# Optimization experiments

Hardware: AMD Instinct MI355X
Metric: run time of the kernel (lower is better)

## Reference

```python
import jax, jax.numpy as jnp
import numpy as np

N_FFT = 512
HOP = 256
FS = 16000
D_INTER = 0.04
C_SOUND = 343.0
SOURCE_NUM = 2
EST_NUM = 4      # TF snapshots for the spatial covariance
T_START = 120    # starting frame of the snapshots
EPS = 1e-8
N_ANGLES = 361   # theta in [-90, 90] deg
T_SAMPLES = 3200000
N_MICS = 4


def _stft(xc):
    """xc: (C, T) real -> X: (C, F, n_frames) complex64.
    Matches torch.stft(center=True, pad_mode='reflect', onesided=True)
    with window = hann(N_FFT, periodic=True) ** 0.5.
    """
    n = jnp.arange(N_FFT, dtype=xc.dtype)
    win = jnp.sqrt(0.5 * (1.0 - jnp.cos(2.0 * jnp.pi * n / N_FFT)))  # hann^0.5
    pad = N_FFT // 2
    xp = jnp.pad(xc, ((0, 0), (pad, pad)), mode='reflect')
    n_frames = 1 + xc.shape[1] // HOP
    idx = jnp.arange(n_frames)[:, None] * HOP + jnp.arange(N_FFT)[None, :]
    frames = xp[:, idx] * win                     # (C, n_frames, N_FFT)
    X = jnp.fft.rfft(frames, axis=-1)             # (C, n_frames, F)
    return jnp.swapaxes(X, 1, 2)                  # (C, F, n_frames)


def setup_inputs() -> dict:
    key = jax.random.key(0)
    x = jax.random.normal(key, (T_SAMPLES, N_MICS), dtype=jnp.float32)
    return {"x": x}


def reference(x) -> jnp.ndarray:
    # ---- multi-channel STFT ----
    X = _stft(x.T)                                # (M, F, T_frames) complex64
    M = X.shape[0]

    # ---- spatial covariance from EST_NUM snapshots (vectorized over bins) ----
    Xs = X[:, :, T_START:T_START + EST_NUM]       # (M, F, EST_NUM)
    spt = jnp.einsum('mft,nft->fmn', Xs, jnp.conj(Xs)) / EST_NUM  # (F, M, M) Hermitian

    # ---- noise subspace via Hermitian eigendecomposition ----
    # eigh returns ascending eigenvalues; take the M-SOURCE_NUM smallest
    # (noise) eigenvectors, i.e. descending order then columns SOURCE_NUM:.
    _, V = jnp.linalg.eigh(spt)                   # (F, M, M)
    noise = V[:, :, ::-1][:, :, SOURCE_NUM:]      # (F, M, M-SOURCE_NUM)

    # ---- spatial spectrum, fully batched over all 361 angles ----
    f_analog = jnp.linspace(0.0, FS / 2, N_FFT // 2 + 1, dtype=jnp.float32)
    theta = jnp.deg2rad(jnp.linspace(-90.0, 90.0, N_ANGLES, dtype=jnp.float32))
    mics = jnp.arange(M, dtype=jnp.float32)
    # phase: (A, F, M)
    phase = (2.0 * jnp.pi * D_INTER / C_SOUND) * (
        jnp.sin(theta)[:, None, None] * f_analog[None, :, None] * mics[None, None, :]
    )
    steer = jnp.exp(-1j * phase).astype(jnp.complex64)            # (A, F, M)
    mid = jnp.einsum('afm,fmk->afk', steer, noise)                # (A, F, K)
    val = jnp.sum(mid.real ** 2 + mid.imag ** 2, axis=-1)         # (A, F)
    spt_spec = jnp.mean(1.0 / (val + EPS), axis=1)                # (A,)
    return spt_spec
```

## Files before the change

kernel.cpp:

```cpp
#include <hip/hip_runtime.h>
#include <math.h>

#define NFFT   512
#define HOP    256
#define NFREQ  257
#define NMIC   4
#define NEST   4
#define TSTART 120
#define NANG   361

static constexpr double PI_D = 3.14159265358979323846;
static constexpr float  PI_F = 3.14159265358979323846f;

__global__ __launch_bounds__(512)
void stft_kernel(const float* __restrict__ x,
                 float* __restrict__ part_re,
                 float* __restrict__ part_im) {
    int b = blockIdx.x;
    int chunk = b >> 4;
    int m = (b >> 2) & 3;
    int t = b & 3;
    int tid = threadIdx.x;

    __shared__ float ct[512];
    __shared__ float st[512];
    __shared__ float v[128];

    {
        float ang = (2.0f * PI_F / 512.0f) * (float)tid;
        float s, c;
        sincosf(ang, &s, &c);
        ct[tid] = c;
        st[tid] = s;
    }
    if (tid < 128) {
        int n = chunk * 128 + tid;
        long base = ((long)(TSTART + t - 1) * HOP) * NMIC + m;
        v[tid] = x[base + (long)n * NMIC] * sinf(PI_F * (float)n / 512.0f);
    }
    __syncthreads();

    int f = tid;
    if (f >= NFREQ) return;
    int n0 = chunk * 128;
    int k = (f * n0) & 511;
    float re = 0.0f, im = 0.0f;
#pragma unroll 4
    for (int j = 0; j < 128; ++j) {
        float vn = v[j];
        re += vn * ct[k];
        im -= vn * st[k];
        k = (k + f) & 511;
    }
    int id = f * 16 + m * 4 + t;
    part_re[chunk * 4112 + id] = re;
    part_im[chunk * 4112 + id] = im;
}

__global__ __launch_bounds__(64)
void eig_kernel(const float* __restrict__ part_re,
                const float* __restrict__ part_im,
                double* __restrict__ pre,
                double* __restrict__ pim) {
    int f = blockIdx.x * blockDim.x + threadIdx.x;
    if (f >= NFREQ) return;

    double Xr[4][4], Xi[4][4];
#pragma unroll
    for (int m = 0; m < 4; ++m)
#pragma unroll
        for (int t = 0; t < 4; ++t) {
            int id = f * 16 + m * 4 + t;
            Xr[m][t] = (double)part_re[id] + (double)part_re[4112 + id]
                     + (double)part_re[2 * 4112 + id] + (double)part_re[3 * 4112 + id];
            Xi[m][t] = (double)part_im[id] + (double)part_im[4112 + id]
                     + (double)part_im[2 * 4112 + id] + (double)part_im[3 * 4112 + id];
        }

    double Ar[4][4], Ai[4][4];
#pragma unroll
    for (int m = 0; m < 4; ++m)
#pragma unroll
        for (int n = 0; n < 4; ++n) {
            double rr = 0.0, ii = 0.0;
#pragma unroll
            for (int t = 0; t < 4; ++t) {
                rr += Xr[m][t] * Xr[n][t] + Xi[m][t] * Xi[n][t];
                ii += Xi[m][t] * Xr[n][t] - Xr[m][t] * Xi[n][t];
            }
            Ar[m][n] = rr;
            Ai[m][n] = ii;
        }

    double Vr[4][4] = {{1,0,0,0},{0,1,0,0},{0,0,1,0},{0,0,0,1}};
    double Vi[4][4] = {{0,0,0,0},{0,0,0,0},{0,0,0,0},{0,0,0,0}};

    for (int sweep = 0; sweep < 6; ++sweep) {
#pragma unroll
        for (int p = 0; p < 3; ++p)
#pragma unroll
            for (int q = p + 1; q < 4; ++q) {
                double ar = Ar[p][q], ai = Ai[p][q];
                double rmag = sqrt(ar * ar + ai * ai);
                if (rmag < 1e-280) continue;
                double inv = 1.0 / rmag;
                double er = ar * inv, ei = ai * inv;
                double tau = (Ar[q][q] - Ar[p][p]) * (0.5 * inv);
                double t_ = (tau >= 0.0 ? 1.0 : -1.0) /
                            (fabs(tau) + sqrt(1.0 + tau * tau));
                double c = 1.0 / sqrt(1.0 + t_ * t_);
                double s = t_ * c;
#pragma unroll
                for (int k = 0; k < 4; ++k) {
                    double apr = Ar[k][p], api = Ai[k][p];
                    double aqr = Ar[k][q], aqi = Ai[k][q];
                    double tr = er * aqr + ei * aqi;
                    double ti = er * aqi - ei * aqr;
                    Ar[k][p] = c * apr - s * tr;
                    Ai[k][p] = c * api - s * ti;
                    double ur = er * apr - ei * api;
                    double ui = er * api + ei * apr;
                    Ar[k][q] = s * ur + c * aqr;
                    Ai[k][q] = s * ui + c * aqi;
                }
#pragma unroll
                for (int k = 0; k < 4; ++k) {
                    double apr = Ar[p][k], api = Ai[p][k];
                    double aqr = Ar[q][k], aqi = Ai[q][k];
                    double tr = er * aqr - ei * aqi;
                    double ti = er * aqi + ei * aqr;
                    Ar[p][k] = c * apr - s * tr;
                    Ai[p][k] = c * api - s * ti;
                    double ur = er * apr + ei * api;
                    double ui = er * api - ei * apr;
                    Ar[q][k] = s * ur + c * aqr;
                    Ai[q][k] = s * ui + c * aqi;
                }
#pragma unroll
                for (int k = 0; k < 4; ++k) {
                    double apr = Vr[k][p], api = Vi[k][p];
                    double aqr = Vr[k][q], aqi = Vi[k][q];
                    double tr = er * aqr + ei * aqi;
                    double ti = er * aqi - ei * aqr;
                    Vr[k][p] = c * apr - s * tr;
                    Vi[k][p] = c * api - s * ti;
                    double ur = er * apr - ei * api;
                    double ui = er * api + ei * apr;
                    Vr[k][q] = s * ur + c * aqr;
                    Vi[k][q] = s * ui + c * aqi;
                }
            }
    }

    double dd[4] = {Ar[0][0], Ar[1][1], Ar[2][2], Ar[3][3]};
    double w[4];
#pragma unroll
    for (int j = 0; j < 4; ++j) {
        int rank = 0;
#pragma unroll
        for (int k = 0; k < 4; ++k) {
            if (k == j) continue;
            bool less = (dd[k] < dd[j]) || (dd[k] == dd[j] && k < j);
            rank += less ? 1 : 0;
        }
        w[j] = (rank < 2) ? 1.0 : 0.0;
    }

#pragma unroll
    for (int m = 0; m < 4; ++m)
#pragma unroll
        for (int n = 0; n < 4; ++n) {
            double rr = 0.0, ii = 0.0;
#pragma unroll
            for (int j = 0; j < 4; ++j) {
                rr += w[j] * (Vr[m][j] * Vr[n][j] + Vi[m][j] * Vi[n][j]);
                ii += w[j] * (Vi[m][j] * Vr[n][j] - Vr[m][j] * Vi[n][j]);
            }
            pre[f * 16 + m * 4 + n] = rr;
            pim[f * 16 + m * 4 + n] = ii;
        }
}

__global__ __launch_bounds__(512)
void music_kernel(const double* __restrict__ pre,
                  const double* __restrict__ pim,
                  float* __restrict__ out) {
    int a = blockIdx.x;
    int f = threadIdx.x;
    double r = 0.0;
    if (f < NFREQ) {
        double theta = (-90.0 + 0.5 * (double)a) * PI_D / 180.0;
        double freq = 31.25 * (double)f;
        double phi = 2.0 * PI_D * 0.04 / 343.0 * sin(theta) * freq;
        const double* Pr = pre + f * 16;
        const double* Pi = pim + f * 16;
        double s1, c1;
        sincos(phi, &s1, &c1);
        double c2 = c1 * c1 - s1 * s1;
        double s2 = 2.0 * s1 * c1;
        double c3 = c1 * c2 - s1 * s2;
        double s3 = s1 * c2 + c1 * s2;
        double val = Pr[0] + Pr[5] + Pr[10] + Pr[15]
            + 2.0 * ( c1 * (Pr[1] + Pr[6] + Pr[11]) - s1 * (Pi[1] + Pi[6] + Pi[11])
                    + c2 * (Pr[2] + Pr[7])          - s2 * (Pi[2] + Pi[7])
                    + c3 * Pr[3]                    - s3 * Pi[3] );
        r = 1.0 / (val + 1e-8);
    }
    __shared__ double sm[512];
    sm[threadIdx.x] = r;
    __syncthreads();
    for (int st = 256; st > 0; st >>= 1) {
        if (threadIdx.x < st) sm[threadIdx.x] += sm[threadIdx.x + st];
        __syncthreads();
    }
    if (threadIdx.x == 0) out[a] = (float)(sm[0] / (double)NFREQ);
}

extern "C" void kernel_launch(void* const* d_in, const int* in_sizes, int n_in,
                              void* d_out, int out_size, void* d_ws, size_t ws_size,
                              hipStream_t stream) {
    const float* x = (const float*)d_in[0];
    float* out = (float*)d_out;

    float*  part_re = (float*)d_ws;
    float*  part_im = part_re + 4 * 4112;
    double* pre     = (double*)((char*)d_ws + 2 * 4 * 4112 * sizeof(float));
    double* pim     = pre + 4112;

    stft_kernel<<<64, 512, 0, stream>>>(x, part_re, part_im);
    eig_kernel<<<(NFREQ + 63) / 64, 64, 0, stream>>>(part_re, part_im, pre, pim);
    music_kernel<<<NANG, 512, 0, stream>>>(pre, pim, out);
}
```

Baseline: 115.8 us.

## Switch eig and MUSIC to fp32, compact coefficients, use wave shuffle reductions

Converts the Jacobi eigensolver and the spatial spectrum kernel from double to single precision, replacing a branchy skip with select-based masking. The eig kernel now emits 7 diagonal-sum coefficients per bin instead of the full 4x4 projector, so the MUSIC kernel loads two float4s per bin. The MUSIC block shrinks to 320 threads and reduces with wave shuffles rather than a shared-memory tree, and STFT twiddles are packed into float2. The fp32 Jacobi with near-degenerate covariance (rank 4 from 4 snapshots) risks accuracy loss in the noise subspace.

```diff
diff --git a/kernel.cpp b/kernel.cpp
--- a/kernel.cpp
+++ b/kernel.cpp
@@ -5,7 +5,6 @@
 #define HOP    256
 #define NFREQ  257
 #define NMIC   4
-#define NEST   4
 #define TSTART 120
 #define NANG   361
 
@@ -22,16 +21,14 @@
     int t = b & 3;
     int tid = threadIdx.x;
 
-    __shared__ float ct[512];
-    __shared__ float st[512];
-    __shared__ float v[128];
+    __shared__ float2 tw[512];
+    __shared__ float  v[128];
 
     {
         float ang = (2.0f * PI_F / 512.0f) * (float)tid;
         float s, c;
         sincosf(ang, &s, &c);
-        ct[tid] = c;
-        st[tid] = s;
+        tw[tid] = make_float2(c, s);
     }
     if (tid < 128) {
         int n = chunk * 128 + tid;
@@ -42,14 +39,14 @@
 
     int f = tid;
     if (f >= NFREQ) return;
-    int n0 = chunk * 128;
-    int k = (f * n0) & 511;
+    int k = (f * (chunk * 128)) & 511;
     float re = 0.0f, im = 0.0f;
 #pragma unroll 4
     for (int j = 0; j < 128; ++j) {
         float vn = v[j];
-        re += vn * ct[k];
-        im -= vn * st[k];
+        float2 cs = tw[k];
+        re += vn * cs.x;
+        im -= vn * cs.y;
         k = (k + f) & 511;
     }
     int id = f * 16 + m * 4 + t;
@@ -60,29 +57,28 @@
 __global__ __launch_bounds__(64)
 void eig_kernel(const float* __restrict__ part_re,
                 const float* __restrict__ part_im,
-                double* __restrict__ pre,
-                double* __restrict__ pim) {
+                float* __restrict__ coef) {
     int f = blockIdx.x * blockDim.x + threadIdx.x;
     if (f >= NFREQ) return;
 
-    double Xr[4][4], Xi[4][4];
+    float Xr[4][4], Xi[4][4];
 #pragma unroll
     for (int m = 0; m < 4; ++m)
 #pragma unroll
         for (int t = 0; t < 4; ++t) {
             int id = f * 16 + m * 4 + t;
-            Xr[m][t] = (double)part_re[id] + (double)part_re[4112 + id]
-                     + (double)part_re[2 * 4112 + id] + (double)part_re[3 * 4112 + id];
-            Xi[m][t] = (double)part_im[id] + (double)part_im[4112 + id]
-                     + (double)part_im[2 * 4112 + id] + (double)part_im[3 * 4112 + id];
+            Xr[m][t] = part_re[id] + part_re[4112 + id]
+                     + part_re[2 * 4112 + id] + part_re[3 * 4112 + id];
+            Xi[m][t] = part_im[id] + part_im[4112 + id]
+                     + part_im[2 * 4112 + id] + part_im[3 * 4112 + id];
         }
 
-    double Ar[4][4], Ai[4][4];
+    float Ar[4][4], Ai[4][4];
 #pragma unroll
     for (int m = 0; m < 4; ++m)
 #pragma unroll
         for (int n = 0; n < 4; ++n) {
-            double rr = 0.0, ii = 0.0;
+            float rr = 0.0f, ii = 0.0f;
 #pragma unroll
             for (int t = 0; t < 4; ++t) {
                 rr += Xr[m][t] * Xr[n][t] + Xi[m][t] * Xi[n][t];
@@ -92,68 +88,69 @@
             Ai[m][n] = ii;
         }
 
-    double Vr[4][4] = {{1,0,0,0},{0,1,0,0},{0,0,1,0},{0,0,0,1}};
-    double Vi[4][4] = {{0,0,0,0},{0,0,0,0},{0,0,0,0},{0,0,0,0}};
+    float Vr[4][4] = {{1,0,0,0},{0,1,0,0},{0,0,1,0},{0,0,0,1}};
+    float Vi[4][4] = {{0,0,0,0},{0,0,0,0},{0,0,0,0},{0,0,0,0}};
 
     for (int sweep = 0; sweep < 6; ++sweep) {
 #pragma unroll
         for (int p = 0; p < 3; ++p)
 #pragma unroll
             for (int q = p + 1; q < 4; ++q) {
-                double ar = Ar[p][q], ai = Ai[p][q];
-                double rmag = sqrt(ar * ar + ai * ai);
-                if (rmag < 1e-280) continue;
-                double inv = 1.0 / rmag;
-                double er = ar * inv, ei = ai * inv;
-                double tau = (Ar[q][q] - Ar[p][p]) * (0.5 * inv);
-                double t_ = (tau >= 0.0 ? 1.0 : -1.0) /
-                            (fabs(tau) + sqrt(1.0 + tau * tau));
-                double c = 1.0 / sqrt(1.0 + t_ * t_);
-                double s = t_ * c;
+                float ar = Ar[p][q], ai = Ai[p][q];
+                float n2 = ar * ar + ai * ai;
+                bool ok = n2 > 1e-24f;
+                float n2s = ok ? n2 : 1.0f;
+                float inv = 1.0f / sqrtf(n2s);
+                float er = ar * inv, ei = ai * inv;
+                float tau = (Ar[q][q] - Ar[p][p]) * (0.5f * inv * (ok ? 1.0f : 0.0f));
+                float t_ = (tau >= 0.0f ? 1.0f : -1.0f) /
+                           (fabsf(tau) + sqrtf(1.0f + tau * tau));
+                float c = ok ? 1.0f / sqrtf(1.0f + t_ * t_) : 1.0f;
+                float s = ok ? t_ * c : 0.0f;
 #pragma unroll
                 for (int k = 0; k < 4; ++k) {
-                    double apr = Ar[k][p], api = Ai[k][p];
-                    double aqr = Ar[k][q], aqi = Ai[k][q];
-                    double tr = er * aqr + ei * aqi;
-                    double ti = er * aqi - ei * aqr;
+                    float apr = Ar[k][p], api = Ai[k][p];
+                    float aqr = Ar[k][q], aqi = Ai[k][q];
+                    float tr = er * aqr + ei * aqi;
+                    float ti = er * aqi - ei * aqr;
                     Ar[k][p] = c * apr - s * tr;
                     Ai[k][p] = c * api - s * ti;
-                    double ur = er * apr - ei * api;
-                    double ui = er * api + ei * apr;
+                    float ur = er * apr - ei * api;
+                    float ui = er * api + ei * apr;
                     Ar[k][q] = s * ur + c * aqr;
                     Ai[k][q] = s * ui + c * aqi;
                 }
 #pragma unroll
                 for (int k = 0; k < 4; ++k) {
-                    double apr = Ar[p][k], api = Ai[p][k];
-                    double aqr = Ar[q][k], aqi = Ai[q][k];
-                    double tr = er * aqr - ei * aqi;
-                    double ti = er * aqi + ei * aqr;
+                    float apr = Ar[p][k], api = Ai[p][k];
+                    float aqr = Ar[q][k], aqi = Ai[q][k];
+                    float tr = er * aqr - ei * aqi;
+                    float ti = er * aqi + ei * aqr;
                     Ar[p][k] = c * apr - s * tr;
                     Ai[p][k] = c * api - s * ti;
-                    double ur = er * apr + ei * api;
-                    double ui = er * api - ei * apr;
+                    float ur = er * apr + ei * api;
+                    float ui = er * api - ei * apr;
                     Ar[q][k] = s * ur + c * aqr;
                     Ai[q][k] = s * ui + c * aqi;
                 }
 #pragma unroll
                 for (int k = 0; k < 4; ++k) {
-                    double apr = Vr[k][p], api = Vi[k][p];
-                    double aqr = Vr[k][q], aqi = Vi[k][q];
-                    double tr = er * aqr + ei * aqi;
-                    double ti = er * aqi - ei * aqr;
+                    float apr = Vr[k][p], api = Vi[k][p];
+                    float aqr = Vr[k][q], aqi = Vi[k][q];
+                    float tr = er * aqr + ei * aqi;
+                    float ti = er * aqi - ei * aqr;
                     Vr[k][p] = c * apr - s * tr;
                     Vi[k][p] = c * api - s * ti;
-                    double ur = er * apr - ei * api;
-                    double ui = er * api + ei * apr;
+                    float ur = er * apr - ei * api;
+                    float ui = er * api + ei * apr;
                     Vr[k][q] = s * ur + c * aqr;
                     Vi[k][q] = s * ui + c * aqi;
                 }
             }
     }
 
-    double dd[4] = {Ar[0][0], Ar[1][1], Ar[2][2], Ar[3][3]};
-    double w[4];
+    float dd[4] = {Ar[0][0], Ar[1][1], Ar[2][2], Ar[3][3]};
+    float w[4];
 #pragma unroll
     for (int j = 0; j < 4; ++j) {
         int rank = 0;
@@ -163,57 +160,67 @@
             bool less = (dd[k] < dd[j]) || (dd[k] == dd[j] && k < j);
             rank += less ? 1 : 0;
         }
-        w[j] = (rank < 2) ? 1.0 : 0.0;
-    }
-
-#pragma unroll
-    for (int m = 0; m < 4; ++m)
-#pragma unroll
-        for (int n = 0; n < 4; ++n) {
-            double rr = 0.0, ii = 0.0;
-#pragma unroll
-            for (int j = 0; j < 4; ++j) {
-                rr += w[j] * (Vr[m][j] * Vr[n][j] + Vi[m][j] * Vi[n][j]);
-                ii += w[j] * (Vi[m][j] * Vr[n][j] - Vr[m][j] * Vi[n][j]);
-            }
-            pre[f * 16 + m * 4 + n] = rr;
-            pim[f * 16 + m * 4 + n] = ii;
-        }
-}
-
-__global__ __launch_bounds__(512)
-void music_kernel(const double* __restrict__ pre,
-                  const double* __restrict__ pim,
+        w[j] = (rank < 2) ? 1.0f : 0.0f;
+    }
+
+    float s1r = 0.f, s1i = 0.f, s2r = 0.f, s2i = 0.f, s3r = 0.f, s3i = 0.f, trc = 0.f;
+#pragma unroll
+    for (int j = 0; j < 4; ++j) {
+        float wj = w[j];
+        s1r += wj * (Vr[0][j]*Vr[1][j] + Vi[0][j]*Vi[1][j]
+                   + Vr[1][j]*Vr[2][j] + Vi[1][j]*Vi[2][j]
+                   + Vr[2][j]*Vr[3][j] + Vi[2][j]*Vi[3][j]);
+        s1i += wj * (Vi[0][j]*Vr[1][j] - Vr[0][j]*Vi[1][j]
+                   + Vi[1][j]*Vr[2][j] - Vr[1][j]*Vi[2][j]
+                   + Vi[2][j]*Vr[3][j] - Vr[2][j]*Vi[3][j]);
+        s2r += wj * (Vr[0][j]*Vr[2][j] + Vi[0][j]*Vi[2][j]
+                   + Vr[1][j]*Vr[3][j] + Vi[1][j]*Vi[3][j]);
+        s2i += wj * (Vi[0][j]*Vr[2][j] - Vr[0][j]*Vi[2][j]
+                   + Vi[1][j]*Vr[3][j] - Vr[1][j]*Vi[3][j]);
+        s3r += wj * (Vr[0][j]*Vr[3][j] + Vi[0][j]*Vi[3][j]);
+        s3i += wj * (Vi[0][j]*Vr[3][j] - Vr[0][j]*Vi[3][j]);
+        trc += wj * (Vr[0][j]*Vr[0][j] + Vi[0][j]*Vi[0][j]
+                   + Vr[1][j]*Vr[1][j] + Vi[1][j]*Vi[1][j]
+                   + Vr[2][j]*Vr[2][j] + Vi[2][j]*Vi[2][j]
+                   + Vr[3][j]*Vr[3][j] + Vi[3][j]*Vi[3][j]);
+    }
+    float* cf = coef + f * 8;
+    cf[0] = s1r; cf[1] = s1i; cf[2] = s2r; cf[3] = s2i;
+    cf[4] = s3r; cf[5] = s3i; cf[6] = trc; cf[7] = 0.0f;
+}
+
+__global__ __launch_bounds__(320)
+void music_kernel(const float* __restrict__ coef,
                   float* __restrict__ out) {
     int a = blockIdx.x;
-    int f = threadIdx.x;
-    double r = 0.0;
-    if (f < NFREQ) {
-        double theta = (-90.0 + 0.5 * (double)a) * PI_D / 180.0;
-        double freq = 31.25 * (double)f;
-        double phi = 2.0 * PI_D * 0.04 / 343.0 * sin(theta) * freq;
-        const double* Pr = pre + f * 16;
-        const double* Pi = pim + f * 16;
-        double s1, c1;
-        sincos(phi, &s1, &c1);
-        double c2 = c1 * c1 - s1 * s1;
-        double s2 = 2.0 * s1 * c1;
-        double c3 = c1 * c2 - s1 * s2;
-        double s3 = s1 * c2 + c1 * s2;
-        double val = Pr[0] + Pr[5] + Pr[10] + Pr[15]
-            + 2.0 * ( c1 * (Pr[1] + Pr[6] + Pr[11]) - s1 * (Pi[1] + Pi[6] + Pi[11])
-                    + c2 * (Pr[2] + Pr[7])          - s2 * (Pi[2] + Pi[7])
-                    + c3 * Pr[3]                    - s3 * Pi[3] );
-        r = 1.0 / (val + 1e-8);
-    }
-    __shared__ double sm[512];
-    sm[threadIdx.x] = r;
+    int tid = threadIdx.x;
+    float r = 0.0f;
+    if (tid < NFREQ) {
+        const float4* cf4 = (const float4*)(coef + tid * 8);
+        float4 cA = cf4[0];
+        float4 cB = cf4[1];
+        float theta = (-90.0f + 0.5f * (float)a) * (PI_F / 180.0f);
+        float freq = 31.25f * (float)tid;
+        float phi = (float)(2.0 * PI_D * 0.04 / 343.0) * sinf(theta) * freq;
+        float s1, c1;
+        sincosf(phi, &s1, &c1);
+        float c2 = c1 * c1 - s1 * s1;
+        float s2 = 2.0f * s1 * c1;
+        float c3 = c1 * c2 - s1 * s2;
+        float s3 = s1 * c2 + c1 * s2;
+        float val = cB.z + 2.0f * (c1 * cA.x - s1 * cA.y
+                                 + c2 * cA.z - s2 * cA.w
+                                 + c3 * cB.x - s3 * cB.y);
+        r = 1.0f / (val + 1e-8f);
+    }
+#pragma unroll
+    for (int off = 32; off > 0; off >>= 1)
+        r += __shfl_down(r, off, 64);
+    __shared__ float ps[5];
+    if ((tid & 63) == 0) ps[tid >> 6] = r;
     __syncthreads();
-    for (int st = 256; st > 0; st >>= 1) {
-        if (threadIdx.x < st) sm[threadIdx.x] += sm[threadIdx.x + st];
-        __syncthreads();
-    }
-    if (threadIdx.x == 0) out[a] = (float)(sm[0] / (double)NFREQ);
+    if (tid == 0)
+        out[a] = (ps[0] + ps[1] + ps[2] + ps[3] + ps[4]) / 257.0f;
 }
 
 extern "C" void kernel_launch(void* const* d_in, const int* in_sizes, int n_in,
@@ -222,12 +229,11 @@
     const float* x = (const float*)d_in[0];
     float* out = (float*)d_out;
 
-    float*  part_re = (float*)d_ws;
-    float*  part_im = part_re + 4 * 4112;
-    double* pre     = (double*)((char*)d_ws + 2 * 4 * 4112 * sizeof(float));
-    double* pim     = pre + 4112;
+    float* part_re = (float*)d_ws;
+    float* part_im = part_re + 4 * 4112;
+    float* coef    = part_im + 4 * 4112;
 
     stft_kernel<<<64, 512, 0, stream>>>(x, part_re, part_im);
-    eig_kernel<<<(NFREQ + 63) / 64, 64, 0, stream>>>(part_re, part_im, pre, pim);
-    music_kernel<<<NANG, 512, 0, stream>>>(pre, pim, out);
-}
+    eig_kernel<<<(NFREQ + 63) / 64, 64, 0, stream>>>(part_re, part_im, coef);
+    music_kernel<<<NANG, 320, 0, stream>>>(coef, out);
+}
```

Result: faster. 108.5 us (-6.3%).
